# Optimization experiments

Hardware: AMD Instinct MI355X
Metric: run time of the kernel (lower is better)

## Reference

```python
import jax, jax.numpy as jnp
import numpy as np

BN_EPS = 1e-5  # torch BatchNorm1d default


def setup_inputs() -> dict:
    key = jax.random.key(0)
    k = jax.random.split(key, 5)
    B, D, L = 4096, 4096, 4  # batch, width, num layers (3 hidden + 1 output)
    x = jax.random.normal(k[0], (B, D), dtype=jnp.float32)
    # Per-layer Linear weights stored as [L, in, out]; scaled like xavier-ish init.
    W = jax.random.normal(k[1], (L, D, D), dtype=jnp.float32) * (1.0 / np.sqrt(D))
    b = jax.random.normal(k[2], (L, D), dtype=jnp.float32) * 0.01
    gamma = jax.random.uniform(k[3], (L, D), dtype=jnp.float32, minval=0.5, maxval=1.5)
    beta = jax.random.normal(k[4], (L, D), dtype=jnp.float32) * 0.1
    return {"x": x, "W": W, "b": b, "gamma": gamma, "beta": beta}


def _layer(h, W_l, b_l, gamma_l, beta_l):
    # one big GEMM replaces the per-neuron GEMV loop + stack
    h = h @ W_l + b_l  # [B, out]
    # BatchNorm1d, training mode: biased batch stats over the batch dim
    mu = jnp.mean(h, axis=0)
    var = jnp.var(h, axis=0)
    h = (h - mu) * jax.lax.rsqrt(var + BN_EPS) * gamma_l + beta_l
    return jax.nn.relu(h)


def reference(x, W, b, gamma, beta):
    out = x
    for l in range(W.shape[0]):  # small fixed layer count
        out = _layer(out, W[l], b[l], gamma[l], beta[l])
    # nn.Softmax(dim=0): softmax over the batch dimension, as in the original
    return jax.nn.softmax(out, axis=0)
```

## Files before the change

kernel.cpp:

```cpp
#include <hip/hip_runtime.h>
#include <stdint.h>

#define DIMD 4096
#define DIMB 4096
#define NLAYER 4
#define NT (DIMD / 64)

typedef unsigned short u16;
typedef __attribute__((ext_vector_type(8))) unsigned short us8;
typedef __attribute__((ext_vector_type(4))) float f32x4;
typedef __attribute__((ext_vector_type(8))) __bf16 bf16x8;

__device__ __forceinline__ u16 f2bf(float f) {
    union { float f; uint32_t u; } v; v.f = f;
    return (u16)((v.u + 0x7fffu + ((v.u >> 16) & 1u)) >> 16);
}
__device__ __forceinline__ float bf2f(u16 u) {
    union { uint32_t u; float f; } v; v.u = ((uint32_t)u) << 16;
    return v.f;
}

__global__ void k_cvt(const float* __restrict__ in, u16* __restrict__ out) {
    int i = (blockIdx.x * 256 + threadIdx.x) * 4;
    float4 v = *reinterpret_cast<const float4*>(in + i);
    ushort4 r;
    r.x = f2bf(v.x); r.y = f2bf(v.y); r.z = f2bf(v.z); r.w = f2bf(v.w);
    *reinterpret_cast<ushort4*>(out + i) = r;
}

__global__ void k_trans(const float* __restrict__ W, u16* __restrict__ Wt) {
    __shared__ float tile[64][65];
    const int t = threadIdx.x;
    const size_t loff = (size_t)blockIdx.z * DIMD * DIMD;
    const int n0 = blockIdx.x * 64, k0 = blockIdx.y * 64;
    const int kr = t >> 4, c4 = (t & 15) * 4;
    #pragma unroll
    for (int r = 0; r < 4; ++r) {
        float4 v = *reinterpret_cast<const float4*>(W + loff + (size_t)(k0 + kr + r * 16) * DIMD + n0 + c4);
        tile[kr + r * 16][c4 + 0] = v.x;
        tile[kr + r * 16][c4 + 1] = v.y;
        tile[kr + r * 16][c4 + 2] = v.z;
        tile[kr + r * 16][c4 + 3] = v.w;
    }
    __syncthreads();
    const int nr = t >> 4, k4 = (t & 15) * 4;
    #pragma unroll
    for (int r = 0; r < 4; ++r) {
        int n = nr + r * 16;
        ushort4 o;
        o.x = f2bf(tile[k4 + 0][n]);
        o.y = f2bf(tile[k4 + 1][n]);
        o.z = f2bf(tile[k4 + 2][n]);
        o.w = f2bf(tile[k4 + 3][n]);
        *reinterpret_cast<ushort4*>(Wt + loff + (size_t)(n0 + n) * DIMD + k0 + k4) = o;
    }
}

#define GLD(g, l) __builtin_amdgcn_global_load_lds( \
    (__attribute__((address_space(1))) void*)(g),   \
    (__attribute__((address_space(3))) void*)(l), 16, 0, 0)

#define VMW8 asm volatile("s_waitcnt vmcnt(8)" ::: "memory")
#define VMW0 asm volatile("s_waitcnt vmcnt(0)" ::: "memory")
#define LGKM0 asm volatile("s_waitcnt lgkmcnt(0)" ::: "memory")

__global__ __launch_bounds__(512, 2) void k_gemm(
        const u16* __restrict__ A, const u16* __restrict__ Bt,
        const float* __restrict__ bias, u16* __restrict__ H,
        float* __restrict__ Hf,
        float* __restrict__ csum, float* __restrict__ csum2) {
    __shared__ __attribute__((aligned(16))) u16 As[2 * 256 * 64];
    __shared__ __attribute__((aligned(16))) u16 Bs[2 * 256 * 64];
    const int tid = threadIdx.x;
    const int lane = tid & 63, wv = tid >> 6;
    const int wm = wv >> 2, wn = wv & 3;
    const int bm = blockIdx.y, bn = blockIdx.x;
    const int lr = lane & 15, lk = lane >> 4;

    const int r0 = tid >> 3;
    const int cswz = (tid & 7) ^ (r0 & 7);
    const u16* gA = A  + (size_t)(bm * 256 + r0) * DIMD + cswz * 8;
    const u16* gB = Bt + (size_t)(bn * 256 + r0) * DIMD + cswz * 8;

#define STAGE_A(h, t, buf) do { \
    const u16* _s = gA + (size_t)(h) * 128 * DIMD + (size_t)(t) * 64; \
    u16* _d = As + (buf) * 16384 + (h) * 8192 + wv * 512; \
    GLD(_s, _d); GLD(_s + (size_t)64 * DIMD, _d + 4096); \
} while (0)
#define STAGE_B(h, t, buf) do { \
    const u16* _s = gB + (size_t)(h) * 128 * DIMD + (size_t)(t) * 64; \
    u16* _d = Bs + (buf) * 16384 + (h) * 8192 + wv * 512; \
    GLD(_s, _d); GLD(_s + (size_t)64 * DIMD, _d + 4096); \
} while (0)

    int aoff[4][2], boff[2][2];
    #pragma unroll
    for (int mf = 0; mf < 4; ++mf)
        #pragma unroll
        for (int ks = 0; ks < 2; ++ks) {
            int row = wm * 128 + mf * 16 + lr;
            aoff[mf][ks] = row * 64 + ((ks * 4 + lk) ^ (row & 7)) * 8;
        }
    #pragma unroll
    for (int nf = 0; nf < 2; ++nf)
        #pragma unroll
        for (int ks = 0; ks < 2; ++ks) {
            int row = wn * 64 + nf * 16 + lr;
            boff[nf][ks] = row * 64 + ((ks * 4 + lk) ^ (row & 7)) * 8;
        }

    f32x4 acc[8][4] = {};
    bf16x8 a[4][2], b0[2][2], b1[2][2];

#define READ_ALO(Ab) _Pragma("unroll") for (int mf = 0; mf < 4; ++mf) \
    _Pragma("unroll") for (int ks = 0; ks < 2; ++ks) \
        a[mf][ks] = *reinterpret_cast<const bf16x8*>((Ab) + aoff[mf][ks])
#define READ_AHI(Ab) _Pragma("unroll") for (int mf = 0; mf < 4; ++mf) \
    _Pragma("unroll") for (int ks = 0; ks < 2; ++ks) \
        a[mf][ks] = *reinterpret_cast<const bf16x8*>((Ab) + 4096 + aoff[mf][ks])
#define READ_B0(Bb) _Pragma("unroll") for (int nf = 0; nf < 2; ++nf) \
    _Pragma("unroll") for (int ks = 0; ks < 2; ++ks) \
        b0[nf][ks] = *reinterpret_cast<const bf16x8*>((Bb) + boff[nf][ks])
#define READ_B1(Bb) _Pragma("unroll") for (int nf = 0; nf < 2; ++nf) \
    _Pragma("unroll") for (int ks = 0; ks < 2; ++ks) \
        b1[nf][ks] = *reinterpret_cast<const bf16x8*>((Bb) + 2048 + boff[nf][ks])
#define MFMA_Q(MO, B, NO) _Pragma("unroll") for (int mf = 0; mf < 4; ++mf) \
    _Pragma("unroll") for (int nf = 0; nf < 2; ++nf) \
    _Pragma("unroll") for (int ks = 0; ks < 2; ++ks) \
        acc[(MO) + mf][(NO) + nf] = __builtin_amdgcn_mfma_f32_16x16x32_bf16( \
            a[mf][ks], B[nf][ks], acc[(MO) + mf][(NO) + nf], 0, 0, 0)

#define TILE(CUR, TN, PF, WEND) do { \
    const u16* Ab = As + (CUR) * 16384; \
    const u16* Bb = Bs + (CUR) * 16384; \
    READ_ALO(Ab); READ_B0(Bb); \
    __builtin_amdgcn_s_barrier(); \
    LGKM0; \
    __builtin_amdgcn_s_setprio(1); \
    MFMA_Q(0, b0, 0); \
    __builtin_amdgcn_s_setprio(0); \
    __builtin_amdgcn_s_barrier(); \
    READ_B1(Bb); \
    __builtin_amdgcn_s_barrier(); \
    LGKM0; \
    __builtin_amdgcn_s_setprio(1); \
    MFMA_Q(0, b1, 2); \
    __builtin_amdgcn_s_setprio(0); \
    __builtin_amdgcn_s_barrier(); \
    READ_AHI(Ab); \
    if (PF) { STAGE_B(0, TN, CUR); STAGE_B(1, TN, CUR); } \
    __builtin_amdgcn_s_barrier(); \
    LGKM0; \
    __builtin_amdgcn_s_setprio(1); \
    MFMA_Q(4, b1, 2); \
    __builtin_amdgcn_s_setprio(0); \
    __builtin_amdgcn_s_barrier(); \
    if (PF) { STAGE_A(0, TN, CUR); STAGE_A(1, TN, CUR); } \
    __builtin_amdgcn_s_setprio(1); \
    MFMA_Q(4, b0, 0); \
    __builtin_amdgcn_s_setprio(0); \
    WEND; \
    __builtin_amdgcn_s_barrier(); \
} while (0)

    STAGE_B(0, 0, 0); STAGE_B(1, 0, 0); STAGE_A(0, 0, 0); STAGE_A(1, 0, 0);
    STAGE_B(0, 1, 1); STAGE_B(1, 1, 1); STAGE_A(0, 1, 1); STAGE_A(1, 1, 1);
    VMW8;
    __builtin_amdgcn_s_barrier();

    for (int tt = 0; tt < NT - 2; tt += 2) {
        TILE(0, tt + 2, true, VMW8);
        TILE(1, tt + 3, true, VMW8);
    }
    TILE(0, 0, false, VMW0);
    TILE(1, 0, false, VMW0);

    #pragma unroll
    for (int nh = 0; nh < 2; ++nh)
        #pragma unroll
        for (int nf = 0; nf < 2; ++nf) {
            int n = nh * 2 + nf;
            int col = bn * 256 + wn * 64 + n * 16 + lr;
            float bv = bias[col];
            float s1 = 0.f, s2 = 0.f;
            #pragma unroll
            for (int m = 0; m < 8; ++m)
                #pragma unroll
                for (int r = 0; r < 4; ++r) {
                    float v = acc[m][n][r] + bv;
                    acc[m][n][r] = v;
                    s1 += v; s2 += v * v;
                }
            s1 += __shfl_xor(s1, 16); s1 += __shfl_xor(s1, 32);
            s2 += __shfl_xor(s2, 16); s2 += __shfl_xor(s2, 32);
            if (lk == 0) {
                atomicAdd(&csum[col], s1);
                atomicAdd(&csum2[col], s2);
            }
        }

    float* Ls = reinterpret_cast<float*>(As) + wv * 1088;
    const int erow = lane >> 3, ecol = (lane & 7) * 8;
    #pragma unroll
    for (int mf = 0; mf < 8; ++mf) {
        #pragma unroll
        for (int n = 0; n < 4; ++n)
            #pragma unroll
            for (int r = 0; r < 4; ++r)
                Ls[(lk * 4 + r) * 68 + n * 16 + lr] = acc[mf][n][r];
        LGKM0;
        #pragma unroll
        for (int g = 0; g < 2; ++g) {
            int rowloc = erow + g * 8;
            size_t gidx = (size_t)(bm * 256 + wm * 128 + mf * 16 + rowloc) * DIMD
                        + bn * 256 + wn * 64 + ecol;
            const float* src = Ls + rowloc * 68 + ecol;
            if (Hf) {
                float4 v0, v1;
                v0.x = src[0]; v0.y = src[1]; v0.z = src[2]; v0.w = src[3];
                v1.x = src[4]; v1.y = src[5]; v1.z = src[6]; v1.w = src[7];
                *reinterpret_cast<float4*>(Hf + gidx) = v0;
                *reinterpret_cast<float4*>(Hf + gidx + 4) = v1;
            } else {
                us8 o;
                #pragma unroll
                for (int c = 0; c < 8; ++c) o[c] = f2bf(src[c]);
                *reinterpret_cast<us8*>(H + gidx) = o;
            }
        }
        LGKM0;
    }
#undef TILE
#undef STAGE_A
#undef STAGE_B
}

__global__ void k_norm(const u16* __restrict__ H, const float* __restrict__ sum,
                       const float* __restrict__ sum2, const float* __restrict__ gamma,
                       const float* __restrict__ beta, u16* __restrict__ o) {
    int j = (blockIdx.x * 256 + threadIdx.x) * 8;
    int i0 = blockIdx.y * 32;
    float s[8], tt[8];
    #pragma unroll
    for (int q = 0; q < 2; ++q) {
        float4 sm = *reinterpret_cast<const float4*>(sum + j + q * 4);
        float4 s2 = *reinterpret_cast<const float4*>(sum2 + j + q * 4);
        float4 gm = *reinterpret_cast<const float4*>(gamma + j + q * 4);
        float4 bt = *reinterpret_cast<const float4*>(beta + j + q * 4);
        #pragma unroll
        for (int c = 0; c < 4; ++c) {
            float mu = (&sm.x)[c] * (1.0f / DIMB);
            float var = (&s2.x)[c] * (1.0f / DIMB) - mu * mu;
            s[q * 4 + c] = (&gm.x)[c] * rsqrtf(var + 1e-5f);
            tt[q * 4 + c] = (&bt.x)[c] - mu * s[q * 4 + c];
        }
    }
    for (int i = i0; i < i0 + 32; ++i) {
        us8 h = *reinterpret_cast<const us8*>(H + (size_t)i * DIMD + j);
        us8 r;
        #pragma unroll
        for (int c = 0; c < 8; ++c)
            r[c] = f2bf(fmaxf(bf2f(h[c]) * s[c] + tt[c], 0.0f));
        *reinterpret_cast<us8*>(o + (size_t)i * DIMD + j) = r;
    }
}

__global__ void k_esum(const float* __restrict__ H, const float* __restrict__ sum,
                       const float* __restrict__ sum2, const float* __restrict__ gamma,
                       const float* __restrict__ beta, float* __restrict__ esum) {
    int j = (blockIdx.x * 256 + threadIdx.x) * 4;
    int i0 = blockIdx.y * 32;
    float4 sm = *reinterpret_cast<const float4*>(sum + j);
    float4 s2 = *reinterpret_cast<const float4*>(sum2 + j);
    float4 gm = *reinterpret_cast<const float4*>(gamma + j);
    float4 bt = *reinterpret_cast<const float4*>(beta + j);
    float s[4], tt[4], acc[4] = {0.f, 0.f, 0.f, 0.f};
    #pragma unroll
    for (int c = 0; c < 4; ++c) {
        float mu = (&sm.x)[c] * (1.0f / DIMB);
        float var = (&s2.x)[c] * (1.0f / DIMB) - mu * mu;
        s[c] = (&gm.x)[c] * rsqrtf(var + 1e-5f);
        tt[c] = (&bt.x)[c] - mu * s[c];
    }
    for (int i = i0; i < i0 + 32; ++i) {
        float4 h = *reinterpret_cast<const float4*>(H + (size_t)i * DIMD + j);
        #pragma unroll
        for (int c = 0; c < 4; ++c)
            acc[c] += __expf(fmaxf((&h.x)[c] * s[c] + tt[c], 0.0f));
    }
    #pragma unroll
    for (int c = 0; c < 4; ++c) atomicAdd(&esum[j + c], acc[c]);
}

__global__ void k_final(float* __restrict__ H, const float* __restrict__ sum,
                        const float* __restrict__ sum2, const float* __restrict__ gamma,
                        const float* __restrict__ beta, const float* __restrict__ esum) {
    int j = (blockIdx.x * 256 + threadIdx.x) * 4;
    int i0 = blockIdx.y * 32;
    float4 sm = *reinterpret_cast<const float4*>(sum + j);
    float4 s2 = *reinterpret_cast<const float4*>(sum2 + j);
    float4 gm = *reinterpret_cast<const float4*>(gamma + j);
    float4 bt = *reinterpret_cast<const float4*>(beta + j);
    float4 es = *reinterpret_cast<const float4*>(esum + j);
    float s[4], tt[4], inv[4];
    #pragma unroll
    for (int c = 0; c < 4; ++c) {
        float mu = (&sm.x)[c] * (1.0f / DIMB);
        float var = (&s2.x)[c] * (1.0f / DIMB) - mu * mu;
        s[c] = (&gm.x)[c] * rsqrtf(var + 1e-5f);
        tt[c] = (&bt.x)[c] - mu * s[c];
        inv[c] = 1.0f / (&es.x)[c];
    }
    for (int i = i0; i < i0 + 32; ++i) {
        float4 h = *reinterpret_cast<const float4*>(H + (size_t)i * DIMD + j);
        float4 o;
        #pragma unroll
        for (int c = 0; c < 4; ++c)
            (&o.x)[c] = __expf(fmaxf((&h.x)[c] * s[c] + tt[c], 0.0f)) * inv[c];
        *reinterpret_cast<float4*>(H + (size_t)i * DIMD + j) = o;
    }
}

extern "C" void kernel_launch(void* const* d_in, const int* in_sizes, int n_in,
                              void* d_out, int out_size, void* d_ws, size_t ws_size,
                              hipStream_t stream) {
    (void)in_sizes; (void)n_in; (void)out_size; (void)ws_size;
    const float* x     = (const float*)d_in[0];
    const float* W     = (const float*)d_in[1];
    const float* b     = (const float*)d_in[2];
    const float* gamma = (const float*)d_in[3];
    const float* beta  = (const float*)d_in[4];
    float* out = (float*)d_out;

    char* ws = (char*)d_ws;
    u16*  Abf = (u16*)ws;
    u16*  Wt4 = (u16*)(ws + (size_t)32 * 1024 * 1024);
    u16*  Hbf = (u16*)(ws + (size_t)160 * 1024 * 1024);
    float* stats = (float*)(ws + (size_t)192 * 1024 * 1024);
    hipMemsetAsync(stats, 0, (4 * 8192 + 4096) * sizeof(float), stream);

    k_cvt<<<DIMB * DIMD / 1024, 256, 0, stream>>>(x, Abf);
    k_trans<<<dim3(64, 64, 4), 256, 0, stream>>>(W, Wt4);

    for (int l = 0; l < NLAYER; ++l) {
        float* sum = stats + l * 8192;
        float* sum2 = sum + 4096;
        float* Hf = (l == NLAYER - 1) ? out : nullptr;
        k_gemm<<<dim3(16, 16), 512, 0, stream>>>(Abf, Wt4 + (size_t)l * DIMD * DIMD,
                                                 b + l * DIMD, Hbf, Hf, sum, sum2);
        if (l < NLAYER - 1)
            k_norm<<<dim3(2, 128), 256, 0, stream>>>(Hbf, sum, sum2,
                gamma + l * DIMD, beta + l * DIMD, Abf);
    }
    k_esum<<<dim3(4, 128), 256, 0, stream>>>(out, stats + 3 * 8192, stats + 3 * 8192 + 4096,
        gamma + 3 * DIMD, beta + 3 * DIMD, stats + 32768);
    k_final<<<dim3(4, 128), 256, 0, stream>>>(out, stats + 3 * 8192, stats + 3 * 8192 + 4096,
        gamma + 3 * DIMD, beta + 3 * DIMD, stats + 32768);
}
```

Baseline: 682.0 us.

## Overlap next layer's weight transpose-convert with current GEMM main loop

The standalone transpose/convert kernel now handles only layer 0's weights. Each GEMM launch reads the next layer's fp32 weights in 8-row slices spread across its K loop, converts them to bf16 and writes them transposed into the workspace. The aim is to hide most of the weight-preparation memory traffic behind MFMA compute instead of paying for it upfront. In exchange it adds 8 live registers and extra global loads and scattered writes inside a tightly scheduled GEMM loop, which could disturb the pipelining or occupancy.

```diff
diff --git a/kernel.cpp b/kernel.cpp
--- a/kernel.cpp
+++ b/kernel.cpp
@@ -31,12 +31,11 @@
 __global__ void k_trans(const float* __restrict__ W, u16* __restrict__ Wt) {
     __shared__ float tile[64][65];
     const int t = threadIdx.x;
-    const size_t loff = (size_t)blockIdx.z * DIMD * DIMD;
     const int n0 = blockIdx.x * 64, k0 = blockIdx.y * 64;
     const int kr = t >> 4, c4 = (t & 15) * 4;
     #pragma unroll
     for (int r = 0; r < 4; ++r) {
-        float4 v = *reinterpret_cast<const float4*>(W + loff + (size_t)(k0 + kr + r * 16) * DIMD + n0 + c4);
+        float4 v = *reinterpret_cast<const float4*>(W + (size_t)(k0 + kr + r * 16) * DIMD + n0 + c4);
         tile[kr + r * 16][c4 + 0] = v.x;
         tile[kr + r * 16][c4 + 1] = v.y;
         tile[kr + r * 16][c4 + 2] = v.z;
@@ -52,7 +51,7 @@
         o.y = f2bf(tile[k4 + 1][n]);
         o.z = f2bf(tile[k4 + 2][n]);
         o.w = f2bf(tile[k4 + 3][n]);
-        *reinterpret_cast<ushort4*>(Wt + loff + (size_t)(n0 + n) * DIMD + k0 + k4) = o;
+        *reinterpret_cast<ushort4*>(Wt + (size_t)(n0 + n) * DIMD + k0 + k4) = o;
     }
 }
 
@@ -68,13 +67,15 @@
         const u16* __restrict__ A, const u16* __restrict__ Bt,
         const float* __restrict__ bias, u16* __restrict__ H,
         float* __restrict__ Hf,
-        float* __restrict__ csum, float* __restrict__ csum2) {
+        float* __restrict__ csum, float* __restrict__ csum2,
+        const float* __restrict__ Wn, u16* __restrict__ WtN) {
     __shared__ __attribute__((aligned(16))) u16 As[2 * 256 * 64];
     __shared__ __attribute__((aligned(16))) u16 Bs[2 * 256 * 64];
     const int tid = threadIdx.x;
     const int lane = tid & 63, wv = tid >> 6;
     const int wm = wv >> 2, wn = wv & 3;
     const int bm = blockIdx.y, bn = blockIdx.x;
+    const int bid = bm * 16 + bn;
     const int lr = lane & 15, lk = lane >> 4;
 
     const int r0 = tid >> 3;
@@ -112,6 +113,9 @@
     f32x4 acc[8][4] = {};
     bf16x8 a[4][2], b0[2][2], b1[2][2];
 
+    const int wcol = (bid & 7) * 512 + tid;
+    float wreg[8];
+
 #define READ_ALO(Ab) _Pragma("unroll") for (int mf = 0; mf < 4; ++mf) \
     _Pragma("unroll") for (int ks = 0; ks < 2; ++ks) \
         a[mf][ks] = *reinterpret_cast<const bf16x8*>((Ab) + aoff[mf][ks])
@@ -169,8 +173,29 @@
     __builtin_amdgcn_s_barrier();
 
     for (int tt = 0; tt < NT - 2; tt += 2) {
+        if (Wn) {
+            if ((tt & 3) == 0) {
+                int k0 = (((bid >> 3) << 4) + (tt >> 2)) << 3;
+                const float* src = Wn + (size_t)k0 * DIMD + wcol;
+                #pragma unroll
+                for (int i = 0; i < 8; ++i) wreg[i] = src[(size_t)i * DIMD];
+            } else {
+                int k0 = (((bid >> 3) << 4) + ((tt - 2) >> 2)) << 3;
+                us8 o;
+                #pragma unroll
+                for (int i = 0; i < 8; ++i) o[i] = f2bf(wreg[i]);
+                *reinterpret_cast<us8*>(WtN + (size_t)wcol * DIMD + k0) = o;
+            }
+        }
         TILE(0, tt + 2, true, VMW8);
         TILE(1, tt + 3, true, VMW8);
+    }
+    if (Wn) {
+        int k0 = (((bid >> 3) << 4) + 15) << 3;
+        us8 o;
+        #pragma unroll
+        for (int i = 0; i < 8; ++i) o[i] = f2bf(wreg[i]);
+        *reinterpret_cast<us8*>(WtN + (size_t)wcol * DIMD + k0) = o;
     }
     TILE(0, 0, false, VMW0);
     TILE(1, 0, false, VMW0);
@@ -340,14 +365,17 @@
     hipMemsetAsync(stats, 0, (4 * 8192 + 4096) * sizeof(float), stream);
 
     k_cvt<<<DIMB * DIMD / 1024, 256, 0, stream>>>(x, Abf);
-    k_trans<<<dim3(64, 64, 4), 256, 0, stream>>>(W, Wt4);
+    k_trans<<<dim3(64, 64), 256, 0, stream>>>(W, Wt4);
 
     for (int l = 0; l < NLAYER; ++l) {
         float* sum = stats + l * 8192;
         float* sum2 = sum + 4096;
         float* Hf = (l == NLAYER - 1) ? out : nullptr;
+        const float* Wnext = (l + 1 < NLAYER) ? W + (size_t)(l + 1) * DIMD * DIMD : nullptr;
+        u16* WtNext = Wt4 + (size_t)((l + 1) & 3) * DIMD * DIMD;
         k_gemm<<<dim3(16, 16), 512, 0, stream>>>(Abf, Wt4 + (size_t)l * DIMD * DIMD,
-                                                 b + l * DIMD, Hbf, Hf, sum, sum2);
+                                                 b + l * DIMD, Hbf, Hf, sum, sum2,
+                                                 Wnext, WtNext);
         if (l < NLAYER - 1)
             k_norm<<<dim3(2, 128), 256, 0, stream>>>(Hbf, sum, sum2,
                 gamma + l * DIMD, beta + l * DIMD, Abf);
```

After: 658.1 us, median of 2. -3.5%, faster.
